# Optimization experiments

Measured on AMD Instinct MI355X. Metric: run time of the kernel, lower is better.

The kernel has to match this reference:

```python
import jax, jax.numpy as jnp
import numpy as np

N_NODES = 50000
N_EDGES = 800000
N_GRAPHS = 512
NNF = 32      # num_node_features
EAD = 16      # edge_attr_dim
UD = 32       # u_dim
H = 64        # hidden_dim
OUT = 1


def _w(key, shape, scale=0.05):
    return (jax.random.normal(key, shape, dtype=jnp.float32) * scale)


def setup_inputs() -> dict:
    key = jax.random.key(0)
    ks = iter(jax.random.split(key, 64))
    inp = {
        "x": jax.random.normal(next(ks), (N_NODES, NNF), dtype=jnp.float32),
        "edge_attr": jax.random.normal(next(ks), (N_EDGES, EAD), dtype=jnp.float32),
        "u": jax.random.normal(next(ks), (N_GRAPHS, UD), dtype=jnp.float32),
        # edge MLPs: Linear(EAD,H), ReLU, Linear(H,H)
        "em1_w1": _w(next(ks), (EAD, H)), "em1_b1": jnp.zeros((H,), jnp.float32),
        "em1_w2": _w(next(ks), (H, H)),   "em1_b2": jnp.zeros((H,), jnp.float32),
        "em2_w1": _w(next(ks), (EAD, H)), "em2_b1": jnp.zeros((H,), jnp.float32),
        "em2_w2": _w(next(ks), (H, H)),   "em2_b2": jnp.zeros((H,), jnp.float32),
        # layer-1 GINEConvs (a,b,c stacked on leading axis 3):
        # internal edge projection lin: Linear(H -> NNF); nn: Linear(NNF,H),ReLU,Linear(H,H)
        "c1_lin_w": _w(next(ks), (3, H, NNF)), "c1_lin_b": jnp.zeros((3, NNF), jnp.float32),
        "c1_w1": _w(next(ks), (3, NNF, H)),    "c1_b1": jnp.zeros((3, H), jnp.float32),
        "c1_w2": _w(next(ks), (3, H, H)),      "c1_b2": jnp.zeros((3, H), jnp.float32),
        # layer-2 GINEConvs: lin: Linear(H->H); nn: Linear(H,H),ReLU,Linear(H,H)
        "c2_lin_w": _w(next(ks), (3, H, H)), "c2_lin_b": jnp.zeros((3, H), jnp.float32),
        "c2_w1": _w(next(ks), (3, H, H)),    "c2_b1": jnp.zeros((3, H), jnp.float32),
        "c2_w2": _w(next(ks), (3, H, H)),    "c2_b2": jnp.zeros((3, H), jnp.float32),
        # fusion linears and head
        "lin1_w": _w(next(ks), (3 * H, H)), "lin1_b": jnp.zeros((H,), jnp.float32),
        "lin2_w": _w(next(ks), (3 * H, H)), "lin2_b": jnp.zeros((H,), jnp.float32),
        "fc_w": _w(next(ks), (H + UD, OUT)), "fc_b": jnp.zeros((OUT,), jnp.float32),
        "edge_index": jax.random.randint(next(ks), (2, N_EDGES), 0, N_NODES, dtype=jnp.int64),
        "batch": jnp.sort(jax.random.randint(next(ks), (N_NODES,), 0, N_GRAPHS, dtype=jnp.int64)),
    }
    return inp


def _gine(x, src, dst, ea, lin_w, lin_b, w1, b1, w2, b2):
    # GINEConv (eps=0): out = nn(x + sum_j relu(x_j + lin(e_ij)))
    m = jax.nn.relu(x[src] + ea @ lin_w + lin_b)          # [E, d_x]
    agg = jax.ops.segment_sum(m, dst, num_segments=x.shape[0])
    h = x + agg
    return jax.nn.relu(h @ w1 + b1) @ w2 + b2             # [N, H]


def _triple(x, src, dst, ea, lw, lb, w1, b1, w2, b2):
    # run 3 parallel GINEConvs (a,b,c) and concat features
    outs = jax.vmap(_gine, in_axes=(None, None, None, None, 0, 0, 0, 0, 0, 0))(
        x, src, dst, ea, lw, lb, w1, b1, w2, b2)          # [3, N, H]
    return outs.transpose(1, 0, 2).reshape(x.shape[0], -1)  # [N, 3H]


def reference(x, edge_attr, u,
              em1_w1, em1_b1, em1_w2, em1_b2,
              em2_w1, em2_b1, em2_w2, em2_b2,
              c1_lin_w, c1_lin_b, c1_w1, c1_b1, c1_w2, c1_b2,
              c2_lin_w, c2_lin_b, c2_w1, c2_b1, c2_w2, c2_b2,
              lin1_w, lin1_b, lin2_w, lin2_b, fc_w, fc_b,
              edge_index, batch):
    src, dst = edge_index[0], edge_index[1]
    # layer 1
    ea1 = jax.nn.relu(edge_attr @ em1_w1 + em1_b1) @ em1_w2 + em1_b2
    h = _triple(x, src, dst, ea1, c1_lin_w, c1_lin_b, c1_w1, c1_b1, c1_w2, c1_b2)
    h = jax.nn.relu(h @ lin1_w + lin1_b)                  # [N, H]
    # layer 2
    ea2 = jax.nn.relu(edge_attr @ em2_w1 + em2_b1) @ em2_w2 + em2_b2
    h = _triple(h, src, dst, ea2, c2_lin_w, c2_lin_b, c2_w1, c2_b1, c2_w2, c2_b2)
    h = jax.nn.relu(h @ lin2_w + lin2_b)                  # [N, H]
    # global mean pool per graph
    sums = jax.ops.segment_sum(h, batch, num_segments=N_GRAPHS)
    cnt = jax.ops.segment_sum(jnp.ones((h.shape[0], 1), h.dtype), batch, num_segments=N_GRAPHS)
    pooled = sums / jnp.maximum(cnt, 1.0)                 # [G, H]
    return jnp.concatenate([pooled, u], axis=-1) @ fc_w + fc_b  # [G, 1]
```

## Files before the change

kernel.cpp:

```cpp
#include <hip/hip_runtime.h>
#include <hip/hip_bf16.h>

#define N_NODES  50000
#define N_EDGES  800000
#define N_GRAPHS 512
#define NTILES   3125
#define ETILES   50000
#define CT       4
#define NCHUNKS  (ETILES / CT)

typedef short bf16x8 __attribute__((ext_vector_type(8)));
typedef float f32x4  __attribute__((ext_vector_type(4)));

constexpr size_t B_CNT  = 0;
constexpr size_t ZERO_BYTES = 200192;
constexpr size_t B_OFF  = 200192;
constexpr size_t B_CUR  = 400384;
constexpr size_t B_BSUM = 600576;
constexpr size_t B_SEDGE= 601600;
constexpr size_t B_DSTA = 7001600;
constexpr size_t B_FR2  = 10201600;
constexpr size_t B_AGG  = 10287616;
constexpr size_t B_H1   = 48687616;
constexpr size_t B_H2   = 61487616;
constexpr size_t B_FOLD = 74287616;
constexpr size_t B_FRAG = 74461440;
constexpr int F_V1H = 0;
constexpr int F_B1F = 6144;
constexpr int F_V2H = 6240;
constexpr int F_B2F = 18528;
constexpr int F_U1  = 18720;
constexpr int F_UB1 = 31008;
constexpr int F_U2  = 31072;
constexpr int F_UB2 = 43360;
constexpr int FOLD_TOTAL = 43424;
constexpr int FR_W1E1 = 0;
constexpr int FR_W1E2 = 2048;
constexpr int FR_V1   = 4096;
constexpr int FR_V2   = 10240;
constexpr int FOLD2_TOTAL = 22528;
constexpr int FR3_M1W = 0;
constexpr int FR3_M1U = 6144;
constexpr int FR3_M2W = 18432;
constexpr int FR3_M2U = 30720;
constexpr int FOLD3_TOTAL = 43008;

__device__ inline unsigned short bf16u(float x) {
    unsigned int ua = __float_as_uint(x);
    return (unsigned short)((ua + 0x7FFFu + ((ua >> 16) & 1u)) >> 16);
}
__device__ inline unsigned int packbf2(float a, float b) {
    unsigned int ua = __float_as_uint(a), ub = __float_as_uint(b);
    return ((ua + 0x7FFFu + ((ua >> 16) & 1u)) >> 16) |
           ((ub + 0x7FFFu + ((ub >> 16) & 1u)) & 0xFFFF0000u);
}

__global__ __launch_bounds__(256) void fold_kernel(
    const float* __restrict__ em1_w2, const float* __restrict__ em1_b2,
    const float* __restrict__ em2_w2, const float* __restrict__ em2_b2,
    const float* __restrict__ c1_lin_w, const float* __restrict__ c1_lin_b,
    const float* __restrict__ c2_lin_w, const float* __restrict__ c2_lin_b,
    const float* __restrict__ c1_w2, const float* __restrict__ c1_b2,
    const float* __restrict__ c2_w2, const float* __restrict__ c2_b2,
    const float* __restrict__ lin1_w, const float* __restrict__ lin1_b,
    const float* __restrict__ lin2_w, const float* __restrict__ lin2_b,
    float* __restrict__ fw)
{
    int idx = blockIdx.x * 256 + threadIdx.x;
    if (idx >= FOLD_TOTAL) return;
    int r = idx;
    if (r < 6144) {
        int k = r / 96, c = r % 96, i = c / 32, j = c % 32;
        float s = 0.f;
        for (int m = 0; m < 64; m++) s = fmaf(em1_w2[k * 64 + m], c1_lin_w[i * 2048 + m * 32 + j], s);
        fw[F_V1H + r] = s; return;
    }
    r -= 6144;
    if (r < 96) {
        int i = r / 32, j = r % 32;
        float s = c1_lin_b[r];
        for (int m = 0; m < 64; m++) s = fmaf(em1_b2[m], c1_lin_w[i * 2048 + m * 32 + j], s);
        fw[F_B1F + r] = s; return;
    }
    r -= 96;
    if (r < 12288) {
        int k = r / 192, c = r % 192, i = c / 64, j = c % 64;
        float s = 0.f;
        for (int m = 0; m < 64; m++) s = fmaf(em2_w2[k * 64 + m], c2_lin_w[i * 4096 + m * 64 + j], s);
        fw[F_V2H + r] = s; return;
    }
    r -= 12288;
    if (r < 192) {
        int i = r / 64, j = r % 64;
        float s = c2_lin_b[r];
        for (int m = 0; m < 64; m++) s = fmaf(em2_b2[m], c2_lin_w[i * 4096 + m * 64 + j], s);
        fw[F_B2F + r] = s; return;
    }
    r -= 192;
    if (r < 12288) {
        int i = r / 4096, k = (r / 64) % 64, j = r % 64;
        float s = 0.f;
        for (int m = 0; m < 64; m++) s = fmaf(c1_w2[i * 4096 + k * 64 + m], lin1_w[(i * 64 + m) * 64 + j], s);
        fw[F_U1 + r] = s; return;
    }
    r -= 12288;
    if (r < 64) {
        float s = lin1_b[r];
        for (int i = 0; i < 3; i++)
            for (int m = 0; m < 64; m++) s = fmaf(c1_b2[i * 64 + m], lin1_w[(i * 64 + m) * 64 + r], s);
        fw[F_UB1 + r] = s; return;
    }
    r -= 64;
    if (r < 12288) {
        int i = r / 4096, k = (r / 64) % 64, j = r % 64;
        float s = 0.f;
        for (int m = 0; m < 64; m++) s = fmaf(c2_w2[i * 4096 + k * 64 + m], lin2_w[(i * 64 + m) * 64 + j], s);
        fw[F_U2 + r] = s; return;
    }
    r -= 12288;
    {
        float s = lin2_b[r];
        for (int i = 0; i < 3; i++)
            for (int m = 0; m < 64; m++) s = fmaf(c2_b2[i * 64 + m], lin2_w[(i * 64 + m) * 64 + r], s);
        fw[F_UB2 + r] = s; return;
    }
}

__global__ __launch_bounds__(256) void fold2_kernel(
    const float* __restrict__ em1_w1, const float* __restrict__ em2_w1,
    const float* __restrict__ fw, unsigned short* __restrict__ fr)
{
    int idx = blockIdx.x * 256 + threadIdx.x;
    if (idx >= FOLD2_TOTAL) return;
    if (idx < 4096) {
        const float* w = (idx < 2048) ? em1_w1 : em2_w1;
        int r = idx & 2047;
        int tt = r >> 9, lane = (r >> 3) & 63, j = r & 7;
        int q = lane >> 4, k = q * 8 + j, m = tt * 16 + (lane & 15);
        fr[idx] = (k < 16) ? bf16u(w[k * 64 + m]) : (unsigned short)0;
        return;
    }
    if (idx < 10240) {
        int r = idx - 4096;
        int nt = r / 1024, ka = (r >> 9) & 1, lane = (r >> 3) & 63, j = r & 7;
        int q = lane >> 4;
        int t = 32 * ka + 16 * (j >> 2) + 4 * q + (j & 3);
        int n = nt * 16 + (lane & 15);
        fr[idx] = bf16u(fw[F_V1H + t * 96 + n]);
        return;
    }
    {
        int r = idx - 10240;
        int nt = r / 1024, ka = (r >> 9) & 1, lane = (r >> 3) & 63, j = r & 7;
        int q = lane >> 4;
        int t = 32 * ka + 16 * (j >> 2) + 4 * q + (j & 3);
        int n = nt * 16 + (lane & 15);
        fr[idx] = bf16u(fw[F_V2H + t * 192 + n]);
        return;
    }
}

__global__ __launch_bounds__(256) void fold3_kernel(
    const float* __restrict__ c1_w1, const float* __restrict__ c2_w1,
    const float* __restrict__ fw, unsigned short* __restrict__ fr2)
{
    int idx = blockIdx.x * 256 + threadIdx.x;
    if (idx >= FOLD3_TOTAL) return;
    if (idx < 6144) {
        int i = idx / 2048, r = idx % 2048;
        int tt = r >> 9, lane = (r >> 3) & 63, jj = r & 7;
        int k = (lane >> 4) * 8 + jj, m = tt * 16 + (lane & 15);
        fr2[FR3_M1W + idx] = bf16u(c1_w1[i * 2048 + k * 64 + m]);
        return;
    }
    if (idx < 18432) {
        int r = idx - 6144;
        int i = r / 4096, r2 = r % 4096;
        int b = r2 >> 10, ka = (r2 >> 9) & 1, lane = (r2 >> 3) & 63, jj = r2 & 7;
        int t = 32 * ka + 16 * (jj >> 2) + 4 * (lane >> 4) + (jj & 3);
        int n = b * 16 + (lane & 15);
        fr2[FR3_M1U + r] = bf16u(fw[F_U1 + i * 4096 + t * 64 + n]);
        return;
    }
    if (idx < 30720) {
        int r = idx - 18432;
        int i = r / 4096, r2 = r % 4096;
        int tt = r2 >> 10, ka = (r2 >> 9) & 1, lane = (r2 >> 3) & 63, jj = r2 & 7;
        int k = ka * 32 + (lane >> 4) * 8 + jj, m = tt * 16 + (lane & 15);
        fr2[FR3_M2W + r] = bf16u(c2_w1[i * 4096 + k * 64 + m]);
        return;
    }
    {
        int r = idx - 30720;
        int i = r / 4096, r2 = r % 4096;
        int b = r2 >> 10, ka = (r2 >> 9) & 1, lane = (r2 >> 3) & 63, jj = r2 & 7;
        int t = 32 * ka + 16 * (jj >> 2) + 4 * (lane >> 4) + (jj & 3);
        int n = b * 16 + (lane & 15);
        fr2[FR3_M2U + r] = bf16u(fw[F_U2 + i * 4096 + t * 64 + n]);
        return;
    }
}

__global__ __launch_bounds__(256) void hist_kernel(const int* __restrict__ ei, int* __restrict__ cnt) {
    int e = blockIdx.x * 256 + threadIdx.x;
    if (e < N_EDGES) atomicAdd(&cnt[ei[N_EDGES + e]], 1);
}

__global__ __launch_bounds__(256) void scan1_kernel(const int* __restrict__ cnt,
                                                    int* __restrict__ off, int* __restrict__ bsum) {
    __shared__ int sh[256];
    int t = threadIdx.x, i = blockIdx.x * 256 + t;
    int v = (i < N_NODES) ? cnt[i] : 0;
    sh[t] = v; __syncthreads();
    for (int d = 1; d < 256; d <<= 1) {
        int add = (t >= d) ? sh[t - d] : 0;
        __syncthreads();
        sh[t] += add;
        __syncthreads();
    }
    if (i < N_NODES) off[i] = sh[t] - v;
    if (t == 255) bsum[blockIdx.x] = sh[255];
}

__global__ __launch_bounds__(256) void scan2_kernel(int* __restrict__ bsum) {
    __shared__ int sh[256];
    int t = threadIdx.x;
    int v = (t < 196) ? bsum[t] : 0;
    sh[t] = v; __syncthreads();
    for (int d = 1; d < 256; d <<= 1) {
        int add = (t >= d) ? sh[t - d] : 0;
        __syncthreads();
        sh[t] += add;
        __syncthreads();
    }
    bsum[t] = sh[t] - v;
}

__global__ __launch_bounds__(256) void scan3_kernel(int* __restrict__ off, const int* __restrict__ bsum,
                                                    int* __restrict__ cur) {
    int i = blockIdx.x * 256 + threadIdx.x;
    if (i < N_NODES) {
        int o = off[i] + bsum[i >> 8];
        off[i] = o;
        cur[i] = o;
    }
    if (i == 0) off[N_NODES] = N_EDGES;
}

__global__ __launch_bounds__(256) void scatter_kernel(const int* __restrict__ ei, int* __restrict__ cur,
                                                      int2* __restrict__ sedge, int* __restrict__ dsta) {
    int e = blockIdx.x * 256 + threadIdx.x;
    if (e >= N_EDGES) return;
    int d = ei[N_EDGES + e];
    int p = atomicAdd(&cur[d], 1);
    sedge[p] = make_int2(ei[e], e);
    dsta[p] = d;
}

#define XLOAD(i) const float xv##i = X[(size_t)__builtin_amdgcn_readlane(se.x, i) * XD + xl];
#define WSTEP(i) { \
    const int dnn = __builtin_amdgcn_readlane(dv, i); \
    if (dnn != curd) { \
        if (curd >= 0) { do_flush(!inside); inside = true; } \
        curd = dnn; \
        acc0 = acc1 = acc2 = 0.f; \
    } \
    if constexpr (PK) { \
        const int base = (i) * SW; \
        const unsigned int xr = (unsigned int)((((i) >> 2) & 1) << 4); \
        const unsigned int w0 = Lu[base + (((unsigned)lane) ^ xr)]; \
        const int i1 = (lane < 32) ? (lane + 64) : (lane - 32); \
        const unsigned int w1 = Lu[base + (((unsigned)i1) ^ xr)]; \
        const unsigned int w2 = Lu[base + (((unsigned)(lane + 32)) ^ xr)]; \
        const float q0 = __uint_as_float(w0 << 16); \
        const float q1 = (lane < 32) ? __uint_as_float(w1 << 16) \
                                     : __uint_as_float(w1 & 0xFFFF0000u); \
        const float q2 = __uint_as_float(w2 & 0xFFFF0000u); \
        acc0 += fmaxf(xv##i + q0, 0.f); \
        acc1 += fmaxf(xv##i + q1, 0.f); \
        acc2 += fmaxf(xv##i + q2, 0.f); \
    } else { \
        const int base = (i) * SW; \
        const float q0 = Lf[base + lane]; \
        const float q1 = Lf[base + 64 + (lane & 31)]; \
        acc0 += fmaxf(xv##i + q0, 0.f); \
        if (lane < 32) acc1 += fmaxf(xv##i + q1, 0.f); \
    } \
}

template<int NT, int XD>
__global__ __launch_bounds__(256, 2) void fused_edge_gather(
    const float* __restrict__ edge_attr, const int2* __restrict__ sedge,
    const int* __restrict__ dsta,
    const unsigned short* __restrict__ w1frag, const float* __restrict__ b1,
    const unsigned short* __restrict__ vfrag,  const float* __restrict__ bias2,
    const float* __restrict__ X, float* __restrict__ agg, int nChunks)
{
    constexpr int  C  = NT * 16;
    constexpr bool PK = (NT == 12);
    constexpr int  SW = PK ? (C / 2 + 1) : (C + 2);
    __shared__ unsigned int lds[4 * 16 * SW];
    const int lane = threadIdx.x & 63;
    const int wid  = threadIdx.x >> 6;
    const int col  = lane & 15;
    const int quad = lane >> 4;
    const int cw   = blockIdx.x * 4 + wid;
    if (cw >= nChunks) return;
    unsigned int* Lu = lds + wid * 16 * SW;
    float*        Lf = (float*)Lu;

    bf16x8 w1f[4];
#pragma unroll
    for (int tt = 0; tt < 4; tt++)
        w1f[tt] = *(const bf16x8*)(w1frag + (tt * 64 + lane) * 8);
    float4 b1v[4];
#pragma unroll
    for (int tt = 0; tt < 4; tt++)
        b1v[tt] = *(const float4*)(b1 + tt * 16 + quad * 4);
    float b2v[NT];
#pragma unroll
    for (int nt = 0; nt < NT; nt++) b2v[nt] = bias2[nt * 16 + col];

    const int xl = lane & (XD - 1);
    float acc0 = 0.f, acc1 = 0.f, acc2 = 0.f;
    int  curd  = -1;
    bool inside = false;

    auto do_flush = [&](bool atomicPath) {
        float* row = agg + (size_t)curd * C;
        if (!atomicPath) {
            row[lane] = acc0;
            if constexpr (PK) { row[64 + lane] = acc1; row[128 + lane] = acc2; }
            else { if (lane < 32) row[64 + lane] = acc1; }
        } else {
            atomicAdd(&row[lane], acc0);
            if constexpr (PK) { atomicAdd(&row[64 + lane], acc1); atomicAdd(&row[128 + lane], acc2); }
            else { if (lane < 32) atomicAdd(&row[64 + lane], acc1); }
        }
    };

    const int t0 = cw * CT;
    int2 se = sedge[(size_t)t0 * 16 + col];
    int  dv = dsta[(size_t)t0 * 16 + col];

    for (int ti = 0; ti < CT; ++ti) {
        const int t = t0 + ti;
        const int s = t * 16 + col;
        const int e = se.y;

        uint4 eau = make_uint4(0u, 0u, 0u, 0u);
        if (quad < 2) {
            const float4 v0 = *(const float4*)(edge_attr + (size_t)e * 16 + quad * 8);
            const float4 v1 = *(const float4*)(edge_attr + (size_t)e * 16 + quad * 8 + 4);
            eau.x = packbf2(v0.x, v0.y); eau.y = packbf2(v0.z, v0.w);
            eau.z = packbf2(v1.x, v1.y); eau.w = packbf2(v1.z, v1.w);
        }
        const bf16x8 eaf = __builtin_bit_cast(bf16x8, eau);

        int2 se_n = se; int dv_n = dv;
        if (ti + 1 < CT) { se_n = sedge[s + 16]; dv_n = dsta[s + 16]; }

        f32x4 c1[4];
#pragma unroll
        for (int tt = 0; tt < 4; tt++) {
            f32x4 ci = {b1v[tt].x, b1v[tt].y, b1v[tt].z, b1v[tt].w};
            c1[tt] = __builtin_amdgcn_mfma_f32_16x16x32_bf16(w1f[tt], eaf, ci, 0, 0, 0);
        }
        bf16x8 a2[2];
#pragma unroll
        for (int ka = 0; ka < 2; ka++) {
            uint4 au;
            au.x = packbf2(fmaxf(c1[2 * ka][0], 0.f),     fmaxf(c1[2 * ka][1], 0.f));
            au.y = packbf2(fmaxf(c1[2 * ka][2], 0.f),     fmaxf(c1[2 * ka][3], 0.f));
            au.z = packbf2(fmaxf(c1[2 * ka + 1][0], 0.f), fmaxf(c1[2 * ka + 1][1], 0.f));
            au.w = packbf2(fmaxf(c1[2 * ka + 1][2], 0.f), fmaxf(c1[2 * ka + 1][3], 0.f));
            a2[ka] = __builtin_bit_cast(bf16x8, au);
        }

        XLOAD(0)  XLOAD(1)  XLOAD(2)  XLOAD(3)
        XLOAD(4)  XLOAD(5)  XLOAD(6)  XLOAD(7)
        XLOAD(8)  XLOAD(9)  XLOAD(10) XLOAD(11)
        XLOAD(12) XLOAD(13) XLOAD(14) XLOAD(15)

        if constexpr (PK) {
            const unsigned int xr = (unsigned int)((quad & 1) << 4);
#pragma unroll
            for (int nt = 0; nt < 6; nt++) {
                const bf16x8 va0 = *(const bf16x8*)(vfrag + ((nt * 2 + 0) * 64 + lane) * 8);
                const bf16x8 va1 = *(const bf16x8*)(vfrag + ((nt * 2 + 1) * 64 + lane) * 8);
                f32x4 ca = {b2v[nt], b2v[nt], b2v[nt], b2v[nt]};
                ca = __builtin_amdgcn_mfma_f32_16x16x32_bf16(a2[0], va0, ca, 0, 0, 0);
                ca = __builtin_amdgcn_mfma_f32_16x16x32_bf16(a2[1], va1, ca, 0, 0, 0);
                const bf16x8 vb0 = *(const bf16x8*)(vfrag + (((nt + 6) * 2 + 0) * 64 + lane) * 8);
                const bf16x8 vb1 = *(const bf16x8*)(vfrag + (((nt + 6) * 2 + 1) * 64 + lane) * 8);
                f32x4 cb = {b2v[nt + 6], b2v[nt + 6], b2v[nt + 6], b2v[nt + 6]};
                cb = __builtin_amdgcn_mfma_f32_16x16x32_bf16(a2[0], vb0, cb, 0, 0, 0);
                cb = __builtin_amdgcn_mfma_f32_16x16x32_bf16(a2[1], vb1, cb, 0, 0, 0);
#pragma unroll
                for (int r = 0; r < 4; r++)
                    Lu[(quad * 4 + r) * SW + (((unsigned)(nt * 16 + col)) ^ xr)] =
                        packbf2(ca[r], cb[r]);
            }
        } else {
#pragma unroll
            for (int nt = 0; nt < NT; nt++) {
                const bf16x8 v0 = *(const bf16x8*)(vfrag + ((nt * 2 + 0) * 64 + lane) * 8);
                const bf16x8 v1 = *(const bf16x8*)(vfrag + ((nt * 2 + 1) * 64 + lane) * 8);
                f32x4 c = {b2v[nt], b2v[nt], b2v[nt], b2v[nt]};
                c = __builtin_amdgcn_mfma_f32_16x16x32_bf16(a2[0], v0, c, 0, 0, 0);
                c = __builtin_amdgcn_mfma_f32_16x16x32_bf16(a2[1], v1, c, 0, 0, 0);
#pragma unroll
                for (int r = 0; r < 4; r++)
                    Lf[(quad * 4 + r) * SW + nt * 16 + col] = c[r];
            }
        }

        WSTEP(0)  WSTEP(1)  WSTEP(2)  WSTEP(3)
        WSTEP(4)  WSTEP(5)  WSTEP(6)  WSTEP(7)
        WSTEP(8)  WSTEP(9)  WSTEP(10) WSTEP(11)
        WSTEP(12) WSTEP(13) WSTEP(14) WSTEP(15)

        se = se_n; dv = dv_n;
    }
    do_flush(true);
}
#undef XLOAD
#undef WSTEP

__global__ __launch_bounds__(256) void mlp1_mfma_kernel(
    const float* __restrict__ x, const float* __restrict__ agg1,
    const unsigned short* __restrict__ fr2, const float* __restrict__ c1_b1,
    const float* __restrict__ fw, float* __restrict__ h1)
{
    const int lane = threadIdx.x & 63, wid = threadIdx.x >> 6;
    const int tile = blockIdx.x * 4 + wid;
    if (tile >= NTILES) return;
    const int col = lane & 15, quad = lane >> 4;
    const int node = tile * 16 + col;

    const float4 xa = *(const float4*)(x + (size_t)node * 32 + quad * 8);
    const float4 xb = *(const float4*)(x + (size_t)node * 32 + quad * 8 + 4);

    f32x4 c2[4];
#pragma unroll
    for (int b = 0; b < 4; b++) {
        const float ub = fw[F_UB1 + b * 16 + col];
        c2[b] = {ub, ub, ub, ub};
    }
#pragma unroll
    for (int i = 0; i < 3; i++) {
        const float4 a0 = *(const float4*)(agg1 + (size_t)node * 96 + i * 32 + quad * 8);
        const float4 a1 = *(const float4*)(agg1 + (size_t)node * 96 + i * 32 + quad * 8 + 4);
        uint4 iu;
        iu.x = packbf2(xa.x + a0.x, xa.y + a0.y);
        iu.y = packbf2(xa.z + a0.z, xa.w + a0.w);
        iu.z = packbf2(xb.x + a1.x, xb.y + a1.y);
        iu.w = packbf2(xb.z + a1.z, xb.w + a1.w);
        const bf16x8 inf = __builtin_bit_cast(bf16x8, iu);

        f32x4 c1[4];
#pragma unroll
        for (int tt = 0; tt < 4; tt++) {
            const bf16x8 wf = *(const bf16x8*)(fr2 + FR3_M1W + ((i * 4 + tt) * 64 + lane) * 8);
            const float4 bi = *(const float4*)(c1_b1 + i * 64 + tt * 16 + quad * 4);
            f32x4 ci = {bi.x, bi.y, bi.z, bi.w};
            c1[tt] = __builtin_amdgcn_mfma_f32_16x16x32_bf16(wf, inf, ci, 0, 0, 0);
        }
        bf16x8 a2[2];
#pragma unroll
        for (int ka = 0; ka < 2; ka++) {
            uint4 au;
            au.x = packbf2(fmaxf(c1[2 * ka][0], 0.f),     fmaxf(c1[2 * ka][1], 0.f));
            au.y = packbf2(fmaxf(c1[2 * ka][2], 0.f),     fmaxf(c1[2 * ka][3], 0.f));
            au.z = packbf2(fmaxf(c1[2 * ka + 1][0], 0.f), fmaxf(c1[2 * ka + 1][1], 0.f));
            au.w = packbf2(fmaxf(c1[2 * ka + 1][2], 0.f), fmaxf(c1[2 * ka + 1][3], 0.f));
            a2[ka] = __builtin_bit_cast(bf16x8, au);
        }
#pragma unroll
        for (int b = 0; b < 4; b++)
#pragma unroll
            for (int ka = 0; ka < 2; ka++) {
                const bf16x8 uf = *(const bf16x8*)(fr2 + FR3_M1U + (((i * 4 + b) * 2 + ka) * 64 + lane) * 8);
                c2[b] = __builtin_amdgcn_mfma_f32_16x16x32_bf16(a2[ka], uf, c2[b], 0, 0, 0);
            }
    }
    const int rowb = tile * 16 + quad * 4;
#pragma unroll
    for (int b = 0; b < 4; b++)
#pragma unroll
        for (int r = 0; r < 4; r++)
            h1[(size_t)(rowb + r) * 64 + b * 16 + col] = fmaxf(c2[b][r], 0.f);
}

__global__ __launch_bounds__(256) void mlp2_mfma_kernel(
    const float* __restrict__ h1, const float* __restrict__ agg2,
    const unsigned short* __restrict__ fr2, const float* __restrict__ c2_b1,
    const float* __restrict__ fw, float* __restrict__ h2)
{
    const int lane = threadIdx.x & 63, wid = threadIdx.x >> 6;
    const int tile = blockIdx.x * 4 + wid;
    if (tile >= NTILES) return;
    const int col = lane & 15, quad = lane >> 4;
    const int node = tile * 16 + col;

    float4 hv[4];
#pragma unroll
    for (int p = 0; p < 4; p++)
        hv[p] = *(const float4*)(h1 + (size_t)node * 64 + (p >> 1) * 32 + quad * 8 + (p & 1) * 4);

    f32x4 c2[4];
#pragma unroll
    for (int b = 0; b < 4; b++) {
        const float ub = fw[F_UB2 + b * 16 + col];
        c2[b] = {ub, ub, ub, ub};
    }
#pragma unroll
    for (int i = 0; i < 3; i++) {
        bf16x8 inf[2];
#pragma unroll
        for (int ka = 0; ka < 2; ka++) {
            const float4 a0 = *(const float4*)(agg2 + (size_t)node * 192 + i * 64 + ka * 32 + quad * 8);
            const float4 a1 = *(const float4*)(agg2 + (size_t)node * 192 + i * 64 + ka * 32 + quad * 8 + 4);
            const float4 h0 = hv[ka * 2], h1v = hv[ka * 2 + 1];
            uint4 iu;
            iu.x = packbf2(h0.x + a0.x, h0.y + a0.y);
            iu.y = packbf2(h0.z + a0.z, h0.w + a0.w);
            iu.z = packbf2(h1v.x + a1.x, h1v.y + a1.y);
            iu.w = packbf2(h1v.z + a1.z, h1v.w + a1.w);
            inf[ka] = __builtin_bit_cast(bf16x8, iu);
        }
        f32x4 c1[4];
#pragma unroll
        for (int tt = 0; tt < 4; tt++) {
            const bf16x8 wf0 = *(const bf16x8*)(fr2 + FR3_M2W + (((i * 4 + tt) * 2 + 0) * 64 + lane) * 8);
            const bf16x8 wf1 = *(const bf16x8*)(fr2 + FR3_M2W + (((i * 4 + tt) * 2 + 1) * 64 + lane) * 8);
            const float4 bi = *(const float4*)(c2_b1 + i * 64 + tt * 16 + quad * 4);
            f32x4 ci = {bi.x, bi.y, bi.z, bi.w};
            ci = __builtin_amdgcn_mfma_f32_16x16x32_bf16(wf0, inf[0], ci, 0, 0, 0);
            c1[tt] = __builtin_amdgcn_mfma_f32_16x16x32_bf16(wf1, inf[1], ci, 0, 0, 0);
        }
        bf16x8 a2[2];
#pragma unroll
        for (int ka = 0; ka < 2; ka++) {
            uint4 au;
            au.x = packbf2(fmaxf(c1[2 * ka][0], 0.f),     fmaxf(c1[2 * ka][1], 0.f));
            au.y = packbf2(fmaxf(c1[2 * ka][2], 0.f),     fmaxf(c1[2 * ka][3], 0.f));
            au.z = packbf2(fmaxf(c1[2 * ka + 1][0], 0.f), fmaxf(c1[2 * ka + 1][1], 0.f));
            au.w = packbf2(fmaxf(c1[2 * ka + 1][2], 0.f), fmaxf(c1[2 * ka + 1][3], 0.f));
            a2[ka] = __builtin_bit_cast(bf16x8, au);
        }
#pragma unroll
        for (int b = 0; b < 4; b++)
#pragma unroll
            for (int ka = 0; ka < 2; ka++) {
                const bf16x8 uf = *(const bf16x8*)(fr2 + FR3_M2U + (((i * 4 + b) * 2 + ka) * 64 + lane) * 8);
                c2[b] = __builtin_amdgcn_mfma_f32_16x16x32_bf16(a2[ka], uf, c2[b], 0, 0, 0);
            }
    }
    const int rowb = tile * 16 + quad * 4;
#pragma unroll
    for (int b = 0; b < 4; b++)
#pragma unroll
        for (int r = 0; r < 4; r++)
            h2[(size_t)(rowb + r) * 64 + b * 16 + col] = fmaxf(c2[b][r], 0.f);
}

__global__ __launch_bounds__(256) void pool_kernel(
    const float* __restrict__ h2, const int* __restrict__ batch,
    const float* __restrict__ u, const float* __restrict__ fc_w,
    const float* __restrict__ fc_b, float* __restrict__ out)
{
    __shared__ float red[256];
    const int g = blockIdx.x, t = threadIdx.x;
    int lo = 0, hi = N_NODES;
    while (lo < hi) { int m = (lo + hi) >> 1; if (batch[m] < g) lo = m + 1; else hi = m; }
    int lo2 = lo, hi2 = N_NODES;
    while (lo2 < hi2) { int m = (lo2 + hi2) >> 1; if (batch[m] < g + 1) lo2 = m + 1; else hi2 = m; }

    const int col = t & 63, ch = t >> 6;
    float s = 0.f;
    for (int idx = lo + ch; idx < lo2; idx += 4) s += h2[(size_t)idx * 64 + col];
    red[t] = s;
    __syncthreads();
    if (t < 64) red[t] = red[t] + red[64 + t] + red[128 + t] + red[192 + t];
    __syncthreads();
    if (t == 0) {
        const float inv = 1.f / fmaxf((float)(lo2 - lo), 1.f);
        float sv = fc_b[0];
        for (int j = 0; j < 64; j++) sv = fmaf(red[j] * inv, fc_w[j], sv);
        for (int k = 0; k < 32; k++) sv = fmaf(u[(size_t)g * 32 + k], fc_w[64 + k], sv);
        out[g] = sv;
    }
}

extern "C" void kernel_launch(void* const* d_in, const int* in_sizes, int n_in,
                              void* d_out, int out_size, void* d_ws, size_t ws_size,
                              hipStream_t stream) {
    (void)in_sizes; (void)n_in; (void)out_size; (void)ws_size;
    const float* x        = (const float*)d_in[0];
    const float* edge_attr= (const float*)d_in[1];
    const float* u        = (const float*)d_in[2];
    const float* em1_w1   = (const float*)d_in[3];
    const float* em1_b1   = (const float*)d_in[4];
    const float* em1_w2   = (const float*)d_in[5];
    const float* em1_b2   = (const float*)d_in[6];
    const float* em2_w1   = (const float*)d_in[7];
    const float* em2_b1   = (const float*)d_in[8];
    const float* em2_w2   = (const float*)d_in[9];
    const float* em2_b2   = (const float*)d_in[10];
    const float* c1_lin_w = (const float*)d_in[11];
    const float* c1_lin_b = (const float*)d_in[12];
    const float* c1_w1    = (const float*)d_in[13];
    const float* c1_b1    = (const float*)d_in[14];
    const float* c1_w2    = (const float*)d_in[15];
    const float* c1_b2    = (const float*)d_in[16];
    const float* c2_lin_w = (const float*)d_in[17];
    const float* c2_lin_b = (const float*)d_in[18];
    const float* c2_w1    = (const float*)d_in[19];
    const float* c2_b1    = (const float*)d_in[20];
    const float* c2_w2    = (const float*)d_in[21];
    const float* c2_b2    = (const float*)d_in[22];
    const float* lin1_w   = (const float*)d_in[23];
    const float* lin1_b   = (const float*)d_in[24];
    const float* lin2_w   = (const float*)d_in[25];
    const float* lin2_b   = (const float*)d_in[26];
    const float* fc_w     = (const float*)d_in[27];
    const float* fc_b     = (const float*)d_in[28];
    const int*   ei       = (const int*)d_in[29];
    const int*   batch    = (const int*)d_in[30];

    char* wsb = (char*)d_ws;
    int*   cnt  = (int*)(wsb + B_CNT);
    int*   off  = (int*)(wsb + B_OFF);
    int*   cur  = (int*)(wsb + B_CUR);
    int*   bsum = (int*)(wsb + B_BSUM);
    int2*  sedge= (int2*)(wsb + B_SEDGE);
    int*   dsta = (int*)(wsb + B_DSTA);
    float* agg  = (float*)(wsb + B_AGG);
    float* h1   = (float*)(wsb + B_H1);
    float* h2   = (float*)(wsb + B_H2);
    float* fw   = (float*)(wsb + B_FOLD);
    unsigned short* fr  = (unsigned short*)(wsb + B_FRAG);
    unsigned short* fr2 = (unsigned short*)(wsb + B_FR2);
    float* out  = (float*)d_out;

    (void)hipMemsetAsync(d_ws, 0, ZERO_BYTES, stream);

    fold_kernel<<<(FOLD_TOTAL + 255) / 256, 256, 0, stream>>>(
        em1_w2, em1_b2, em2_w2, em2_b2, c1_lin_w, c1_lin_b, c2_lin_w, c2_lin_b,
        c1_w2, c1_b2, c2_w2, c2_b2, lin1_w, lin1_b, lin2_w, lin2_b, fw);
    fold2_kernel<<<(FOLD2_TOTAL + 255) / 256, 256, 0, stream>>>(em1_w1, em2_w1, fw, fr);
    fold3_kernel<<<(FOLD3_TOTAL + 255) / 256, 256, 0, stream>>>(c1_w1, c2_w1, fw, fr2);

    hist_kernel<<<N_EDGES / 256, 256, 0, stream>>>(ei, cnt);
    scan1_kernel<<<196, 256, 0, stream>>>(cnt, off, bsum);
    scan2_kernel<<<1, 256, 0, stream>>>(bsum);
    scan3_kernel<<<196, 256, 0, stream>>>(off, bsum, cur);
    scatter_kernel<<<N_EDGES / 256, 256, 0, stream>>>(ei, cur, sedge, dsta);

    (void)hipMemsetAsync(wsb + B_AGG, 0, (size_t)N_NODES * 96 * 4, stream);
    fused_edge_gather<6, 32><<<NCHUNKS / 4, 256, 0, stream>>>(
        edge_attr, sedge, dsta, fr + FR_W1E1, em1_b1, fr + FR_V1, fw + F_B1F, x, agg, NCHUNKS);
    mlp1_mfma_kernel<<<(NTILES + 3) / 4, 256, 0, stream>>>(x, agg, fr2, c1_b1, fw, h1);

    (void)hipMemsetAsync(wsb + B_AGG, 0, (size_t)N_NODES * 192 * 4, stream);
    fused_edge_gather<12, 64><<<NCHUNKS / 4, 256, 0, stream>>>(
        edge_attr, sedge, dsta, fr + FR_W1E2, em2_b1, fr + FR_V2, fw + F_B2F, h1, agg, NCHUNKS);
    mlp2_mfma_kernel<<<(NTILES + 3) / 4, 256, 0, stream>>>(h1, agg, fr2, c2_b1, fw, h2);

    pool_kernel<<<N_GRAPHS, 256, 0, stream>>>(h2, batch, u, fc_w, fc_b, out);
}
```

Measured before the change: 479.7 us.

## Split layer-1 edge MLP and gather, storing edge messages in FP8

Layer 1 no longer uses the fused edge-MLP-plus-gather kernel. A standalone MFMA kernel now computes the per-edge 96-wide messages and writes them to a workspace buffer in packed FP8. A per-node gather kernel then walks each node's CSR segment and reduces relu(x[src]+msg) without atomics, which also makes the agg memset unnecessary. This trades the fused kernel's LDS staging and atomic flushes for an extra global round trip of the messages, and FP8 storage adds quantization error. Layer 2 keeps the fused path, now specialised to a non-template kernel.

```diff
diff --git a/kernel.cpp b/kernel.cpp
--- a/kernel.cpp
+++ b/kernel.cpp
@@ -11,6 +11,7 @@
 
 typedef short bf16x8 __attribute__((ext_vector_type(8)));
 typedef float f32x4  __attribute__((ext_vector_type(4)));
+typedef float f32x2  __attribute__((ext_vector_type(2)));
 
 constexpr size_t B_CNT  = 0;
 constexpr size_t ZERO_BYTES = 200192;
@@ -25,6 +26,7 @@
 constexpr size_t B_H2   = 61487616;
 constexpr size_t B_FOLD = 74287616;
 constexpr size_t B_FRAG = 74461440;
+constexpr size_t B_Q    = 74506496;
 constexpr int F_V1H = 0;
 constexpr int F_B1F = 6144;
 constexpr int F_V2H = 6240;
@@ -54,6 +56,12 @@
     return ((ua + 0x7FFFu + ((ua >> 16) & 1u)) >> 16) |
            ((ub + 0x7FFFu + ((ub >> 16) & 1u)) & 0xFFFF0000u);
 }
+__device__ inline unsigned short pkfp8(float a, float b) {
+    return (unsigned short)__builtin_amdgcn_cvt_pk_fp8_f32(a, b, 0, false);
+}
+__device__ inline f32x2 unpkfp8(unsigned short us) {
+    return __builtin_amdgcn_cvt_pk_f32_fp8((int)us, false);
+}
 
 __global__ __launch_bounds__(256) void fold_kernel(
     const float* __restrict__ em1_w2, const float* __restrict__ em1_b2,
@@ -257,7 +265,124 @@
     dsta[p] = d;
 }
 
-#define XLOAD(i) const float xv##i = X[(size_t)__builtin_amdgcn_readlane(se.x, i) * XD + xl];
+template<int NT>
+__global__ __launch_bounds__(256, 2) void edge_mfma_kernel(
+    const float* __restrict__ edge_attr, const int2* __restrict__ sedge,
+    const unsigned short* __restrict__ w1frag, const float* __restrict__ b1,
+    const unsigned short* __restrict__ vfrag,  const float* __restrict__ bias2,
+    unsigned short* __restrict__ qout, int nTiles)
+{
+    const int lane = threadIdx.x & 63;
+    const int wid  = threadIdx.x >> 6;
+    const int col  = lane & 15;
+    const int quad = lane >> 4;
+
+    bf16x8 w1f[4];
+#pragma unroll
+    for (int tt = 0; tt < 4; tt++)
+        w1f[tt] = *(const bf16x8*)(w1frag + (tt * 64 + lane) * 8);
+    bf16x8 vf[NT][2];
+#pragma unroll
+    for (int nt = 0; nt < NT; nt++)
+#pragma unroll
+        for (int ka = 0; ka < 2; ka++)
+            vf[nt][ka] = *(const bf16x8*)(vfrag + ((nt * 2 + ka) * 64 + lane) * 8);
+    float4 b1v[4];
+#pragma unroll
+    for (int tt = 0; tt < 4; tt++)
+        b1v[tt] = *(const float4*)(b1 + tt * 16 + quad * 4);
+    float b2v[NT];
+#pragma unroll
+    for (int nt = 0; nt < NT; nt++) b2v[nt] = bias2[nt * 16 + col];
+
+    const int gw = blockIdx.x * 4 + wid;
+    const int stride = gridDim.x * 4;
+    for (int t = gw; t < nTiles; t += stride) {
+        const int s = t * 16 + col;
+        const int e = sedge[s].y;
+        bf16x8 eaf;
+        uint4 eau = make_uint4(0u, 0u, 0u, 0u);
+        if (quad < 2) {
+            const float4 v0 = *(const float4*)(edge_attr + (size_t)e * 16 + quad * 8);
+            const float4 v1 = *(const float4*)(edge_attr + (size_t)e * 16 + quad * 8 + 4);
+            eau.x = packbf2(v0.x, v0.y); eau.y = packbf2(v0.z, v0.w);
+            eau.z = packbf2(v1.x, v1.y); eau.w = packbf2(v1.z, v1.w);
+        }
+        eaf = __builtin_bit_cast(bf16x8, eau);
+
+        f32x4 c1[4];
+#pragma unroll
+        for (int tt = 0; tt < 4; tt++) {
+            f32x4 ci = {b1v[tt].x, b1v[tt].y, b1v[tt].z, b1v[tt].w};
+            c1[tt] = __builtin_amdgcn_mfma_f32_16x16x32_bf16(w1f[tt], eaf, ci, 0, 0, 0);
+        }
+
+        bf16x8 a2[2];
+#pragma unroll
+        for (int ka = 0; ka < 2; ka++) {
+            uint4 au;
+            au.x = packbf2(fmaxf(c1[2 * ka][0], 0.f),     fmaxf(c1[2 * ka][1], 0.f));
+            au.y = packbf2(fmaxf(c1[2 * ka][2], 0.f),     fmaxf(c1[2 * ka][3], 0.f));
+            au.z = packbf2(fmaxf(c1[2 * ka + 1][0], 0.f), fmaxf(c1[2 * ka + 1][1], 0.f));
+            au.w = packbf2(fmaxf(c1[2 * ka + 1][2], 0.f), fmaxf(c1[2 * ka + 1][3], 0.f));
+            a2[ka] = __builtin_bit_cast(bf16x8, au);
+        }
+
+        f32x4 c2[NT];
+#pragma unroll
+        for (int nt = 0; nt < NT; nt++) {
+            f32x4 ci = {b2v[nt], b2v[nt], b2v[nt], b2v[nt]};
+            ci = __builtin_amdgcn_mfma_f32_16x16x32_bf16(a2[0], vf[nt][0], ci, 0, 0, 0);
+            c2[nt] = __builtin_amdgcn_mfma_f32_16x16x32_bf16(a2[1], vf[nt][1], ci, 0, 0, 0);
+        }
+
+        const size_t rowb = (size_t)t * 16 + quad * 4;
+#pragma unroll
+        for (int b = 0; b < NT / 2; b++) {
+#pragma unroll
+            for (int r = 0; r < 4; r++) {
+                qout[(rowb + r) * (size_t)(NT * 8) + b * 16 + col] =
+                    pkfp8(c2[2 * b][r], c2[2 * b + 1][r]);
+            }
+        }
+    }
+}
+
+__global__ __launch_bounds__(64) void gather1_kernel(
+    const float* __restrict__ x, const int* __restrict__ off, const int2* __restrict__ sedge,
+    const unsigned short* __restrict__ q1, float* __restrict__ agg1)
+{
+    const int n = blockIdx.x, l = threadIdx.x;
+    if (l >= 48) return;
+    const int s0 = off[n], s1 = off[n + 1];
+    const int c = l & 15;
+    const int n1 = (l >> 4) * 32 + c, n2 = n1 + 16;
+    float a0 = 0.f, a1 = 0.f, b0 = 0.f, b1 = 0.f;
+    int s = s0;
+    for (; s + 2 <= s1; s += 2) {
+        const int srcA = sedge[s].x, srcB = sedge[s + 1].x;
+        const unsigned short uA = q1[(size_t)s * 48 + l];
+        const unsigned short uB = q1[(size_t)(s + 1) * 48 + l];
+        const float xA0 = x[(size_t)srcA * 32 + c], xA1 = x[(size_t)srcA * 32 + c + 16];
+        const float xB0 = x[(size_t)srcB * 32 + c], xB1 = x[(size_t)srcB * 32 + c + 16];
+        const f32x2 dA = unpkfp8(uA);
+        const f32x2 dB = unpkfp8(uB);
+        a0 += fmaxf(xA0 + dA.x, 0.f);
+        a1 += fmaxf(xA1 + dA.y, 0.f);
+        b0 += fmaxf(xB0 + dB.x, 0.f);
+        b1 += fmaxf(xB1 + dB.y, 0.f);
+    }
+    if (s < s1) {
+        const int src = sedge[s].x;
+        const f32x2 d = unpkfp8(q1[(size_t)s * 48 + l]);
+        a0 += fmaxf(x[(size_t)src * 32 + c] + d.x, 0.f);
+        a1 += fmaxf(x[(size_t)src * 32 + c + 16] + d.y, 0.f);
+    }
+    agg1[(size_t)n * 96 + n1] = a0 + b0;
+    agg1[(size_t)n * 96 + n2] = a1 + b1;
+}
+
+#define XLOAD(i) const float xv##i = X[(size_t)__builtin_amdgcn_readlane(se.x, i) * 64 + xl];
 #define WSTEP(i) { \
     const int dnn = __builtin_amdgcn_readlane(dv, i); \
     if (dnn != curd) { \
@@ -265,40 +390,30 @@
         curd = dnn; \
         acc0 = acc1 = acc2 = 0.f; \
     } \
-    if constexpr (PK) { \
-        const int base = (i) * SW; \
-        const unsigned int xr = (unsigned int)((((i) >> 2) & 1) << 4); \
-        const unsigned int w0 = Lu[base + (((unsigned)lane) ^ xr)]; \
-        const int i1 = (lane < 32) ? (lane + 64) : (lane - 32); \
-        const unsigned int w1 = Lu[base + (((unsigned)i1) ^ xr)]; \
-        const unsigned int w2 = Lu[base + (((unsigned)(lane + 32)) ^ xr)]; \
-        const float q0 = __uint_as_float(w0 << 16); \
-        const float q1 = (lane < 32) ? __uint_as_float(w1 << 16) \
-                                     : __uint_as_float(w1 & 0xFFFF0000u); \
-        const float q2 = __uint_as_float(w2 & 0xFFFF0000u); \
-        acc0 += fmaxf(xv##i + q0, 0.f); \
-        acc1 += fmaxf(xv##i + q1, 0.f); \
-        acc2 += fmaxf(xv##i + q2, 0.f); \
-    } else { \
-        const int base = (i) * SW; \
-        const float q0 = Lf[base + lane]; \
-        const float q1 = Lf[base + 64 + (lane & 31)]; \
-        acc0 += fmaxf(xv##i + q0, 0.f); \
-        if (lane < 32) acc1 += fmaxf(xv##i + q1, 0.f); \
-    } \
-}
-
-template<int NT, int XD>
-__global__ __launch_bounds__(256, 2) void fused_edge_gather(
+    const int base = (i) * SW; \
+    const unsigned int xr = (unsigned int)((((i) >> 2) & 1) << 4); \
+    const unsigned int w0 = Lu[base + (((unsigned)lane) ^ xr)]; \
+    const int i1 = (lane < 32) ? (lane + 64) : (lane - 32); \
+    const unsigned int w1 = Lu[base + (((unsigned)i1) ^ xr)]; \
+    const unsigned int w2 = Lu[base + (((unsigned)(lane + 32)) ^ xr)]; \
+    const float q0 = __uint_as_float(w0 << 16); \
+    const float q1 = (lane < 32) ? __uint_as_float(w1 << 16) \
+                                 : __uint_as_float(w1 & 0xFFFF0000u); \
+    const float q2 = __uint_as_float(w2 & 0xFFFF0000u); \
+    acc0 += fmaxf(xv##i + q0, 0.f); \
+    acc1 += fmaxf(xv##i + q1, 0.f); \
+    acc2 += fmaxf(xv##i + q2, 0.f); \
+}
+
+__global__ __launch_bounds__(256, 2) void fused_edge_gather2(
     const float* __restrict__ edge_attr, const int2* __restrict__ sedge,
     const int* __restrict__ dsta,
     const unsigned short* __restrict__ w1frag, const float* __restrict__ b1,
     const unsigned short* __restrict__ vfrag,  const float* __restrict__ bias2,
     const float* __restrict__ X, float* __restrict__ agg, int nChunks)
 {
-    constexpr int  C  = NT * 16;
-    constexpr bool PK = (NT == 12);
-    constexpr int  SW = PK ? (C / 2 + 1) : (C + 2);
+    constexpr int C  = 192;
+    constexpr int SW = C / 2 + 1;
     __shared__ unsigned int lds[4 * 16 * SW];
     const int lane = threadIdx.x & 63;
     const int wid  = threadIdx.x >> 6;
@@ -307,7 +422,6 @@
     const int cw   = blockIdx.x * 4 + wid;
     if (cw >= nChunks) return;
     unsigned int* Lu = lds + wid * 16 * SW;
-    float*        Lf = (float*)Lu;
 
     bf16x8 w1f[4];
 #pragma unroll
@@ -317,11 +431,11 @@
 #pragma unroll
     for (int tt = 0; tt < 4; tt++)
         b1v[tt] = *(const float4*)(b1 + tt * 16 + quad * 4);
-    float b2v[NT];
-#pragma unroll
-    for (int nt = 0; nt < NT; nt++) b2v[nt] = bias2[nt * 16 + col];
-
-    const int xl = lane & (XD - 1);
+    float b2v[12];
+#pragma unroll
+    for (int nt = 0; nt < 12; nt++) b2v[nt] = bias2[nt * 16 + col];
+
+    const int xl = lane;
     float acc0 = 0.f, acc1 = 0.f, acc2 = 0.f;
     int  curd  = -1;
     bool inside = false;
@@ -329,13 +443,11 @@
     auto do_flush = [&](bool atomicPath) {
         float* row = agg + (size_t)curd * C;
         if (!atomicPath) {
-            row[lane] = acc0;
-            if constexpr (PK) { row[64 + lane] = acc1; row[128 + lane] = acc2; }
-            else { if (lane < 32) row[64 + lane] = acc1; }
+            row[lane] = acc0; row[64 + lane] = acc1; row[128 + lane] = acc2;
         } else {
             atomicAdd(&row[lane], acc0);
-            if constexpr (PK) { atomicAdd(&row[64 + lane], acc1); atomicAdd(&row[128 + lane], acc2); }
-            else { if (lane < 32) atomicAdd(&row[64 + lane], acc1); }
+            atomicAdd(&row[64 + lane], acc1);
+            atomicAdd(&row[128 + lane], acc2);
         }
     };
 
@@ -382,7 +494,7 @@
         XLOAD(8)  XLOAD(9)  XLOAD(10) XLOAD(11)
         XLOAD(12) XLOAD(13) XLOAD(14) XLOAD(15)
 
-        if constexpr (PK) {
+        {
             const unsigned int xr = (unsigned int)((quad & 1) << 4);
 #pragma unroll
             for (int nt = 0; nt < 6; nt++) {
@@ -400,18 +512,6 @@
                 for (int r = 0; r < 4; r++)
                     Lu[(quad * 4 + r) * SW + (((unsigned)(nt * 16 + col)) ^ xr)] =
                         packbf2(ca[r], cb[r]);
-            }
-        } else {
-#pragma unroll
-            for (int nt = 0; nt < NT; nt++) {
-                const bf16x8 v0 = *(const bf16x8*)(vfrag + ((nt * 2 + 0) * 64 + lane) * 8);
-                const bf16x8 v1 = *(const bf16x8*)(vfrag + ((nt * 2 + 1) * 64 + lane) * 8);
-                f32x4 c = {b2v[nt], b2v[nt], b2v[nt], b2v[nt]};
-                c = __builtin_amdgcn_mfma_f32_16x16x32_bf16(a2[0], v0, c, 0, 0, 0);
-                c = __builtin_amdgcn_mfma_f32_16x16x32_bf16(a2[1], v1, c, 0, 0, 0);
-#pragma unroll
-                for (int r = 0; r < 4; r++)
-                    Lf[(quad * 4 + r) * SW + nt * 16 + col] = c[r];
             }
         }
 
@@ -642,6 +742,7 @@
     float* fw   = (float*)(wsb + B_FOLD);
     unsigned short* fr  = (unsigned short*)(wsb + B_FRAG);
     unsigned short* fr2 = (unsigned short*)(wsb + B_FR2);
+    unsigned short* q1  = (unsigned short*)(wsb + B_Q);
     float* out  = (float*)d_out;
 
     (void)hipMemsetAsync(d_ws, 0, ZERO_BYTES, stream);
@@ -658,13 +759,13 @@
     scan3_kernel<<<196, 256, 0, stream>>>(off, bsum, cur);
     scatter_kernel<<<N_EDGES / 256, 256, 0, stream>>>(ei, cur, sedge, dsta);
 
-    (void)hipMemsetAsync(wsb + B_AGG, 0, (size_t)N_NODES * 96 * 4, stream);
-    fused_edge_gather<6, 32><<<NCHUNKS / 4, 256, 0, stream>>>(
-        edge_attr, sedge, dsta, fr + FR_W1E1, em1_b1, fr + FR_V1, fw + F_B1F, x, agg, NCHUNKS);
+    edge_mfma_kernel<6><<<2048, 256, 0, stream>>>(
+        edge_attr, sedge, fr + FR_W1E1, em1_b1, fr + FR_V1, fw + F_B1F, q1, ETILES);
+    gather1_kernel<<<N_NODES, 64, 0, stream>>>(x, off, sedge, q1, agg);
     mlp1_mfma_kernel<<<(NTILES + 3) / 4, 256, 0, stream>>>(x, agg, fr2, c1_b1, fw, h1);
 
     (void)hipMemsetAsync(wsb + B_AGG, 0, (size_t)N_NODES * 192 * 4, stream);
-    fused_edge_gather<12, 64><<<NCHUNKS / 4, 256, 0, stream>>>(
+    fused_edge_gather2<<<NCHUNKS / 4, 256, 0, stream>>>(
         edge_attr, sedge, dsta, fr + FR_W1E2, em2_b1, fr + FR_V2, fw + F_B2F, h1, agg, NCHUNKS);
     mlp2_mfma_kernel<<<(NTILES + 3) / 4, 256, 0, stream>>>(h1, agg, fr2, c2_b1, fw, h2);
 
```

Result: no change. 486.7 us (+1.5%).
